# Performance work log

Hardware: AMD Instinct MI355X
Metric: run time of the kernel (lower is better)

Reference implementation:

```python
import jax, jax.numpy as jnp
import numpy as np

DIM = 256; HEADS = 8; B = 8; N = 128; MLP_HID = 4 * DIM


def _ln(x, g, b):
    m = x.mean(-1, keepdims=True)
    v = ((x - m) ** 2).mean(-1, keepdims=True)
    return (x - m) / jnp.sqrt(v + 1e-5) * g + b


def _mlp(x, W1, b1, W2, b2):
    return jax.nn.relu(x @ W1 + b1) @ W2 + b2


def setup_inputs():
    key = jax.random.key(0)
    ks = iter(jax.random.split(key, 48))
    def p(*shape):
        return jax.random.normal(next(ks), shape, jnp.float32) * 0.02
    inp = {
        'x': jax.random.normal(next(ks), (B, N, DIM), jnp.float32),
        'y': jax.random.normal(next(ks), (B, N, N, DIM), jnp.float32),
        'heads': HEADS,
    }
    for nm in ['q', 'k', 'v', 'e', 'oe', 'on']:
        inp['W' + nm] = p(DIM, DIM)
        inp['b' + nm] = p(DIM)
    for nm in ['ln1', 'ln3', 'ln4', 'ln5', 'ln6']:
        inp[nm + '_g'] = jnp.ones((DIM,), jnp.float32)
        inp[nm + '_b'] = jnp.zeros((DIM,), jnp.float32)
    inp['m1_W1'] = p(DIM, MLP_HID); inp['m1_b1'] = p(MLP_HID)
    inp['m1_W2'] = p(MLP_HID, DIM); inp['m1_b2'] = p(DIM)
    inp['m2_W1'] = p(DIM, MLP_HID); inp['m2_b1'] = p(MLP_HID)
    inp['m2_W2'] = p(MLP_HID, DIM); inp['m2_b2'] = p(DIM)
    return inp


def reference(x, y, heads, Wq, bq, Wk, bk, Wv, bv, We, be, Woe, boe, Won, bon,
              ln1_g, ln1_b, ln3_g, ln3_b, ln4_g, ln4_b, ln5_g, ln5_b, ln6_g, ln6_b,
              m1_W1, m1_b1, m1_W2, m1_b2, m2_W1, m2_b1, m2_W2, m2_b2):
    b, n, c = x.shape
    dk = c // heads
    x1 = _ln(x, ln1_g, ln1_b)
    q = (x1 @ Wq + bq).reshape(b, n, heads, dk)
    k = (x1 @ Wk + bk).reshape(b, n, heads, dk)
    v = (x1 @ Wv + bv).reshape(b, n, heads, dk)
    e = (y @ We + be).reshape(b, n, n, heads, dk)
    # elementwise QK (not a dot product), edge-modulated: (b,n,n,h,dk)
    attn = (q[:, :, None] * k[:, None]) / jnp.sqrt(jnp.float32(dk))
    attn = attn * (e + 1.0) * e
    edge = attn.reshape(b, n, n, c) @ Woe + boe
    attn = jax.nn.softmax(attn, axis=2)  # softmax over key/node axis
    node = (attn * v[:, None]).sum(axis=2).reshape(b, n, c)
    node = node @ Won + bon
    x2 = _ln(x1 + node, ln3_g, ln3_b)
    y2 = _ln(edge + y, ln4_g, ln4_b)
    x_out = _ln(x2 + _mlp(x2, m1_W1, m1_b1, m1_W2, m1_b2), ln5_g, ln5_b)
    y_out = _ln(y2 + _mlp(y2, m2_W1, m2_b1, m2_W2, m2_b2), ln6_g, ln6_b)
    return (x_out, y_out)
```

## Files before the change

kernel.cpp:

```cpp
#include <hip/hip_runtime.h>
#include <hip/hip_bf16.h>


#define DIMC 256
#define NSEQ 128
#define NB 8
#define HID 1024
#define EROWS (NB * NSEQ * NSEQ)

typedef __attribute__((ext_vector_type(8)))  short short8;
typedef __attribute__((ext_vector_type(16))) float f32x16;
typedef __attribute__((ext_vector_type(4)))  float f32x4;

__device__ __forceinline__ short f2bf(float f) {
    union { float f; unsigned u; } v; v.f = f;
    unsigned r = (v.u + 0x7FFF + ((v.u >> 16) & 1)) >> 16;
    return (short)r;
}
__device__ __forceinline__ float bf2f(short s) {
    union { unsigned u; float f; } v; v.u = ((unsigned)(unsigned short)s) << 16;
    return v.f;
}

__device__ __forceinline__ float wave_sum(float v) {
    #pragma unroll
    for (int o = 32; o; o >>= 1) v += __shfl_xor(v, o, 64);
    return v;
}

__device__ __forceinline__ float block_reduce_sum(float v, float* sc, int t) {
    #pragma unroll
    for (int o = 32; o > 0; o >>= 1) v += __shfl_down(v, o, 64);
    __syncthreads();
    if ((t & 63) == 0) sc[t >> 6] = v;
    __syncthreads();
    return sc[0] + sc[1] + sc[2] + sc[3];
}

__global__ __launch_bounds__(256, 2) void k_ln_qkv(
    const float* __restrict__ X, const float* __restrict__ g, const float* __restrict__ be,
    const float* __restrict__ Wq, const float* __restrict__ bq,
    const float* __restrict__ Wk, const float* __restrict__ bk,
    const float* __restrict__ Wv, const float* __restrict__ bv,
    float* __restrict__ X1, float* __restrict__ Q, float* __restrict__ K, float* __restrict__ V)
{
    __shared__ float xs[DIMC];
    __shared__ float red[4];
    const int t = threadIdx.x;
    const int row = blockIdx.x;
    float v = X[(size_t)row * DIMC + t];
    float mu = block_reduce_sum(v, red, t) * (1.f / DIMC);
    float d = v - mu;
    float var = block_reduce_sum(d * d, red, t) * (1.f / DIMC);
    float x1v = d * rsqrtf(var + 1e-5f) * g[t] + be[t];
    xs[t] = x1v;
    X1[(size_t)row * DIMC + t] = x1v;
    __syncthreads();
    float aq = bq[t], ak = bk[t], av = bv[t];
    #pragma unroll 4
    for (int k2 = 0; k2 < DIMC; ++k2) {
        float xv = xs[k2];
        aq = fmaf(xv, Wq[k2 * DIMC + t], aq);
        ak = fmaf(xv, Wk[k2 * DIMC + t], ak);
        av = fmaf(xv, Wv[k2 * DIMC + t], av);
    }
    Q[(size_t)row * DIMC + t] = aq;
    K[(size_t)row * DIMC + t] = ak;
    V[(size_t)row * DIMC + t] = av;
}

__global__ __launch_bounds__(256) void k_transpose_bf16(
    const float* __restrict__ src, short* __restrict__ dst, int M, int N)
{
    __shared__ short tile[32][33];
    const int t = threadIdx.x, tx = t & 31, ty = t >> 5;
    const int bx = blockIdx.x, by = blockIdx.y;
    #pragma unroll
    for (int r = ty; r < 32; r += 8)
        tile[r][tx] = f2bf(src[(size_t)(by * 32 + r) * N + bx * 32 + tx]);
    __syncthreads();
    #pragma unroll
    for (int r = ty; r < 32; r += 8)
        dst[(size_t)(bx * 32 + r) * M + by * 32 + tx] = tile[tx][r];
}

__global__ __launch_bounds__(256) void k_prep_wc(
    const float* __restrict__ W1, const float* __restrict__ W2, short* __restrict__ Wc)
{
    const int h = blockIdx.x, t = threadIdx.x;
    short* dst = Wc + (size_t)h * 32768;
    const int hh = t & 63, kq = t >> 6;
    for (int k0 = 0; k0 < 256; k0 += 4) {
        const int k = k0 + kq;
        float v = W1[(size_t)k * HID + h * 64 + hh];
        dst[hh * 256 + (((k >> 3) ^ (hh & 7)) << 3) + (k & 7)] = f2bf(v);
    }
    short* dst2 = dst + 16384;
    for (int kk = 0; kk < 64; ++kk) {
        float v = W2[(size_t)(h * 64 + kk) * DIMC + t];
        dst2[t * 64 + (((kk >> 3) ^ (t & 7)) << 3) + (kk & 7)] = f2bf(v);
    }
}

__global__ __launch_bounds__(256, 2) void k_e_attn_m(
    const float* __restrict__ Y, const short* __restrict__ WeT,
    const float* __restrict__ be,
    const float* __restrict__ Q, const float* __restrict__ Kp,
    short* __restrict__ ATTb)
{
    __shared__ __align__(16) short As[64][256];
    const int t = threadIdx.x, w = t >> 6, lane = t & 63;
    const int l31 = lane & 31, kg = lane >> 5;
    const size_t R0 = (size_t)blockIdx.x * 64;

    for (int r = w * 16; r < w * 16 + 16; ++r) {
        float4 y4 = *(const float4*)&Y[(R0 + r) * DIMC + lane * 4];
        short4 s4;
        s4.x = f2bf(y4.x); s4.y = f2bf(y4.y); s4.z = f2bf(y4.z); s4.w = f2bf(y4.w);
        *(short4*)&As[r][(((lane >> 1) ^ (r & 7)) << 3) + (lane & 1) * 4] = s4;
    }
    __syncthreads();

    const int rh = (w & 1) * 32, cbase = (w >> 1) * 128;
    const int sw = l31 & 7;
    f32x16 acc[4];
    #pragma unroll
    for (int a = 0; a < 4; ++a)
        #pragma unroll
        for (int i = 0; i < 16; ++i) acc[a][i] = 0.f;

    #pragma unroll
    for (int ks = 0; ks < 16; ++ks) {
        const int gk = 2 * ks + kg;
        short8 a = *(const short8*)&As[rh + l31][(gk ^ sw) * 8];
        #pragma unroll
        for (int tt = 0; tt < 4; ++tt) {
            short8 b = *(const short8*)&WeT[(size_t)(cbase + tt * 32 + l31) * DIMC + gk * 8];
            acc[tt] = __builtin_amdgcn_mfma_f32_32x32x16_bf16(a, b, acc[tt], 0, 0, 0);
        }
    }

    const int m0 = (int)(R0);
    const int qrow = m0 >> 7, bidx = m0 >> 14, jb = m0 & 127;
    const float isq = 0.17677669529663687f;
    #pragma unroll
    for (int tt = 0; tt < 4; ++tt) {
        const int n = cbase + tt * 32 + l31;
        const float qv = Q[(size_t)qrow * DIMC + n];
        const float bb = be[n];
        #pragma unroll
        for (int i = 0; i < 16; ++i) {
            const int row = rh + 4 * kg + (i & 3) + 8 * (i >> 2);
            const float kv = Kp[(size_t)((bidx << 7) + jb + row) * DIMC + n];
            const float e = acc[tt][i] + bb;
            const float qk = qv * kv * isq;
            ATTb[(size_t)(m0 + row) * DIMC + n] = f2bf(qk * (e + 1.f) * e);
        }
    }
}

__global__ __launch_bounds__(256, 2) void k_edge_m(
    const short* __restrict__ ATTb, const short* __restrict__ WoeT,
    const float* __restrict__ boe, float* __restrict__ EDGE)
{
    __shared__ __align__(16) short As[64][256];
    const int t = threadIdx.x, w = t >> 6, lane = t & 63;
    const int l31 = lane & 31, kg = lane >> 5;
    const size_t R0 = (size_t)blockIdx.x * 64;

    #pragma unroll
    for (int it = 0; it < 8; ++it) {
        const int r = w * 16 + it * 2 + kg;
        short8 v = *(const short8*)&ATTb[(R0 + r) * DIMC + l31 * 8];
        *(short8*)&As[r][((l31 ^ (r & 7))) * 8] = v;
    }
    __syncthreads();

    const int rh = (w & 1) * 32, cbase = (w >> 1) * 128;
    const int sw = l31 & 7;
    f32x16 acc[4];
    #pragma unroll
    for (int a = 0; a < 4; ++a)
        #pragma unroll
        for (int i = 0; i < 16; ++i) acc[a][i] = 0.f;

    #pragma unroll
    for (int ks = 0; ks < 16; ++ks) {
        const int gk = 2 * ks + kg;
        short8 a = *(const short8*)&As[rh + l31][(gk ^ sw) * 8];
        #pragma unroll
        for (int tt = 0; tt < 4; ++tt) {
            short8 b = *(const short8*)&WoeT[(size_t)(cbase + tt * 32 + l31) * DIMC + gk * 8];
            acc[tt] = __builtin_amdgcn_mfma_f32_32x32x16_bf16(a, b, acc[tt], 0, 0, 0);
        }
    }

    const int m0 = (int)(R0);
    #pragma unroll
    for (int tt = 0; tt < 4; ++tt) {
        const int n = cbase + tt * 32 + l31;
        const float bb = boe[n];
        #pragma unroll
        for (int i = 0; i < 16; ++i) {
            const int row = rh + 4 * kg + (i & 3) + 8 * (i >> 2);
            EDGE[(size_t)(m0 + row) * DIMC + n] = acc[tt][i] + bb;
        }
    }
}

__global__ __launch_bounds__(256, 2) void k_node_x(
    const short* __restrict__ ATTb, const float* __restrict__ V,
    const float* __restrict__ X1,
    const float* __restrict__ Won, const float* __restrict__ bon,
    const float* __restrict__ g3, const float* __restrict__ b3,
    const float* __restrict__ W1, const float* __restrict__ b1,
    const float* __restrict__ W2, const float* __restrict__ b2,
    const float* __restrict__ g5, const float* __restrict__ b5,
    float* __restrict__ OUTX)
{
    __shared__ float ns[DIMC];
    __shared__ float x2s[DIMC];
    __shared__ float hs[HID];
    __shared__ float red[4];
    const int t = threadIdx.x;
    const int bi = blockIdx.x;
    const int b = bi >> 7;
    const short* arow = ATTb + (size_t)bi * NSEQ * DIMC + t;
    const float* vbase = V + (size_t)b * NSEQ * DIMC + t;
    float l = 0.f, acc = 0.f;
    #pragma unroll 4
    for (int j = 0; j < NSEQ; ++j) {
        float a = bf2f(arow[(size_t)j * DIMC]);
        float vv = vbase[(size_t)j * DIMC];
        float p = __expf(a);
        l += p;
        acc = fmaf(p, vv, acc);
    }
    ns[t] = acc / l;
    __syncthreads();
    float o = bon[t];
    #pragma unroll 4
    for (int k2 = 0; k2 < DIMC; ++k2) o = fmaf(ns[k2], Won[k2 * DIMC + t], o);
    float resid = X1[(size_t)bi * DIMC + t] + o;
    float mu = block_reduce_sum(resid, red, t) * (1.f / DIMC);
    float d = resid - mu;
    float var = block_reduce_sum(d * d, red, t) * (1.f / DIMC);
    float x2 = d * rsqrtf(var + 1e-5f) * g3[t] + b3[t];
    x2s[t] = x2;
    __syncthreads();
    float4 h = *(const float4*)&b1[t * 4];
    for (int k2 = 0; k2 < DIMC; ++k2) {
        float xv = x2s[k2];
        float4 w = *(const float4*)&W1[(size_t)k2 * HID + t * 4];
        h.x = fmaf(xv, w.x, h.x); h.y = fmaf(xv, w.y, h.y);
        h.z = fmaf(xv, w.z, h.z); h.w = fmaf(xv, w.w, h.w);
    }
    h.x = fmaxf(h.x, 0.f); h.y = fmaxf(h.y, 0.f); h.z = fmaxf(h.z, 0.f); h.w = fmaxf(h.w, 0.f);
    *(float4*)&hs[t * 4] = h;
    __syncthreads();
    float o2 = b2[t];
    #pragma unroll 4
    for (int hh = 0; hh < HID; ++hh) o2 = fmaf(hs[hh], W2[(size_t)hh * DIMC + t], o2);
    float r2 = x2 + o2;
    float mu2 = block_reduce_sum(r2, red, t) * (1.f / DIMC);
    float d2 = r2 - mu2;
    float v2 = block_reduce_sum(d2 * d2, red, t) * (1.f / DIMC);
    OUTX[(size_t)bi * DIMC + t] = d2 * rsqrtf(v2 + 1e-5f) * g5[t] + b5[t];
}

__global__ __launch_bounds__(256, 1) void k_mlp_y6(
    float* __restrict__ EY, const float* __restrict__ Y,
    const float* __restrict__ g4, const float* __restrict__ b4,
    const short* __restrict__ Wc, const float* __restrict__ b1v,
    const float* __restrict__ b2v,
    const float* __restrict__ g6, const float* __restrict__ b6)
{
    __shared__ __align__(16) short Wbuf[2][32768];
    __shared__ __align__(16) short Hscr[4][32][64];
    const int t = threadIdx.x;
    const int w = t >> 6, lane = t & 63;
    const int l31 = lane & 31, kg = lane >> 5;
    const int r7 = l31 & 7;
    const size_t R0 = (size_t)blockIdx.x * 128;
    short* Wb = &Wbuf[0][0];

    {
        const float4 gv = *(const float4*)&g4[lane * 4];
        const float4 bv = *(const float4*)&b4[lane * 4];
        const int gw = lane >> 1;
        for (int rr = 0; rr < 32; ++rr) {
            const int row = w * 32 + rr;
            const float4 e4 = *(const float4*)&EY[(R0 + row) * DIMC + lane * 4];
            const float4 y4v = *(const float4*)&Y[(R0 + row) * DIMC + lane * 4];
            float v0 = e4.x + y4v.x, v1 = e4.y + y4v.y, v2 = e4.z + y4v.z, v3 = e4.w + y4v.w;
            float mu = wave_sum(v0 + v1 + v2 + v3) * (1.f / DIMC);
            float d0 = v0 - mu, d1 = v1 - mu, d2 = v2 - mu, d3 = v3 - mu;
            float var = wave_sum(d0 * d0 + d1 * d1 + d2 * d2 + d3 * d3) * (1.f / DIMC);
            float rs = rsqrtf(var + 1e-5f);
            short4 s4;
            s4.x = f2bf(d0 * rs * gv.x + bv.x);
            s4.y = f2bf(d1 * rs * gv.y + bv.y);
            s4.z = f2bf(d2 * rs * gv.z + bv.z);
            s4.w = f2bf(d3 * rs * gv.w + bv.w);
            *(short4*)&Wb[row * 256 + ((gw ^ (rr & 7)) << 3) + (lane & 1) * 4] = s4;
        }
    }
    short8 af[16];
    {
        const int row = w * 32 + l31;
        #pragma unroll
        for (int s = 0; s < 16; ++s)
            af[s] = *(const short8*)&Wb[row * 256 + (((2 * s + kg) ^ r7) << 3)];
    }

    auto stage = [&](int h, int buf) {
        const char* src = (const char*)Wc + (size_t)h * 65536 + t * 16;
        char* dstb = (char*)&Wbuf[buf][0] + t * 16;
        #pragma unroll
        for (int p = 0; p < 16; ++p) {
            __builtin_amdgcn_global_load_lds(
                (const __attribute__((address_space(1))) unsigned*)(src + p * 4096),
                (__attribute__((address_space(3))) unsigned*)(dstb + p * 4096),
                16, 0, 0);
        }
    };
    stage(0, 1);
    __syncthreads();

    f32x16 acc[8];
    #pragma unroll
    for (int a = 0; a < 8; ++a)
        #pragma unroll
        for (int i = 0; i < 16; ++i) acc[a][i] = 0.f;

    for (int h = 0; h < 16; ++h) {
        const short* Wlds = &Wbuf[1 - (h & 1)][0];
        if (h < 15) stage(h + 1, h & 1);
        const float bb0 = b1v[h * 64 + l31];
        const float bb1 = b1v[h * 64 + 32 + l31];

        f32x16 c1[2];
        #pragma unroll
        for (int a = 0; a < 2; ++a)
            #pragma unroll
            for (int i = 0; i < 16; ++i) c1[a][i] = 0.f;
        #pragma unroll
        for (int s = 0; s < 16; ++s) {
            const int g = ((2 * s + kg) ^ r7) << 3;
            #pragma unroll
            for (int tt = 0; tt < 2; ++tt) {
                short8 b = *(const short8*)&Wlds[(tt * 32 + l31) * 256 + g];
                c1[tt] = __builtin_amdgcn_mfma_f32_32x32x16_bf16(af[s], b, c1[tt], 0, 0, 0);
            }
        }
        #pragma unroll
        for (int tt = 0; tt < 2; ++tt) {
            const int cq = tt * 4 + (l31 >> 3), c7 = l31 & 7;
            const float bb = tt ? bb1 : bb0;
            #pragma unroll
            for (int i = 0; i < 16; ++i) {
                const int row = 4 * kg + (i & 3) + 8 * (i >> 2);
                Hscr[w][row][((cq ^ (row & 7)) << 3) + c7] =
                    f2bf(fmaxf(c1[tt][i] + bb, 0.f));
            }
        }
        #pragma unroll
        for (int s = 0; s < 4; ++s) {
            const int g2 = ((2 * s + kg) ^ r7) << 3;
            short8 hf = *(const short8*)&Hscr[w][l31][g2];
            #pragma unroll
            for (int ct = 0; ct < 8; ++ct) {
                short8 b = *(const short8*)&Wlds[16384 + (ct * 32 + l31) * 64 + g2];
                acc[ct] = __builtin_amdgcn_mfma_f32_32x32x16_bf16(hf, b, acc[ct], 0, 0, 0);
            }
        }
        __syncthreads();
    }

    {
        const int row = w * 32 + l31;
        #pragma unroll
        for (int s = 0; s < 16; ++s)
            *(short8*)&Wb[row * 256 + (((2 * s + kg) ^ r7) << 3)] = af[s];
    }
    #pragma unroll
    for (int ct = 0; ct < 8; ++ct) {
        const int col = ct * 32 + l31;
        const float bb = b2v[col];
        const int cq = col >> 3, c7 = col & 7;
        #pragma unroll
        for (int i = 0; i < 16; ++i) {
            const int row = 4 * kg + (i & 3) + 8 * (i >> 2);
            short yv = Wb[(w * 32 + row) * 256 + ((cq ^ (row & 7)) << 3) + c7];
            acc[ct][i] += bb + bf2f(yv);
        }
    }
    float mus[16], rss[16];
    #pragma unroll
    for (int i = 0; i < 16; ++i) {
        float s = 0.f;
        #pragma unroll
        for (int ct = 0; ct < 8; ++ct) s += acc[ct][i];
        #pragma unroll
        for (int m = 1; m < 32; m <<= 1) s += __shfl_xor(s, m, 64);
        mus[i] = s * (1.f / DIMC);
    }
    #pragma unroll
    for (int i = 0; i < 16; ++i) {
        float v = 0.f;
        #pragma unroll
        for (int ct = 0; ct < 8; ++ct) { float d = acc[ct][i] - mus[i]; v += d * d; }
        #pragma unroll
        for (int m = 1; m < 32; m <<= 1) v += __shfl_xor(v, m, 64);
        rss[i] = rsqrtf(v * (1.f / DIMC) + 1e-5f);
    }
    #pragma unroll
    for (int ct = 0; ct < 8; ++ct) {
        const int col = ct * 32 + l31;
        const float gg = g6[col], bo = b6[col];
        #pragma unroll
        for (int i = 0; i < 16; ++i) {
            const int row = 4 * kg + (i & 3) + 8 * (i >> 2);
            EY[(R0 + w * 32 + row) * DIMC + col] = (acc[ct][i] - mus[i]) * rss[i] * gg + bo;
        }
    }
}

extern "C" void kernel_launch(void* const* d_in, const int* in_sizes, int n_in,
                              void* d_out, int out_size, void* d_ws, size_t ws_size,
                              hipStream_t stream) {
    const float* x    = (const float*)d_in[0];
    const float* y    = (const float*)d_in[1];
    const float* Wq   = (const float*)d_in[3];  const float* bq  = (const float*)d_in[4];
    const float* Wk   = (const float*)d_in[5];  const float* bk  = (const float*)d_in[6];
    const float* Wv   = (const float*)d_in[7];  const float* bv  = (const float*)d_in[8];
    const float* We   = (const float*)d_in[9];  const float* be  = (const float*)d_in[10];
    const float* Woe  = (const float*)d_in[11]; const float* boe = (const float*)d_in[12];
    const float* Won  = (const float*)d_in[13]; const float* bon = (const float*)d_in[14];
    const float* ln1g = (const float*)d_in[15]; const float* ln1b = (const float*)d_in[16];
    const float* ln3g = (const float*)d_in[17]; const float* ln3b = (const float*)d_in[18];
    const float* ln4g = (const float*)d_in[19]; const float* ln4b = (const float*)d_in[20];
    const float* ln5g = (const float*)d_in[21]; const float* ln5b = (const float*)d_in[22];
    const float* ln6g = (const float*)d_in[23]; const float* ln6b = (const float*)d_in[24];
    const float* m1W1 = (const float*)d_in[25]; const float* m1b1 = (const float*)d_in[26];
    const float* m1W2 = (const float*)d_in[27]; const float* m1b2 = (const float*)d_in[28];
    const float* m2W1 = (const float*)d_in[29]; const float* m2b1 = (const float*)d_in[30];
    const float* m2W2 = (const float*)d_in[31]; const float* m2b2 = (const float*)d_in[32];

    float* outx = (float*)d_out;
    float* outy = (float*)d_out + NB * NSEQ * DIMC;

    float* ws  = (float*)d_ws;
    float* X1  = ws;
    float* Q   = ws + 262144;
    float* K   = ws + 524288;
    float* V   = ws + 786432;
    short* wsS = (short*)(ws + 1048576);
    short* WeT  = wsS;
    short* WoeT = wsS + 65536;
    short* Wc   = wsS + 131072;
    short* ATTb = wsS + 655360;

    k_transpose_bf16<<<dim3(8, 8),  256, 0, stream>>>(We,   WeT,  DIMC, DIMC);
    k_transpose_bf16<<<dim3(8, 8),  256, 0, stream>>>(Woe,  WoeT, DIMC, DIMC);
    k_prep_wc<<<16, 256, 0, stream>>>(m2W1, m2W2, Wc);

    k_ln_qkv<<<NB * NSEQ, 256, 0, stream>>>(x, ln1g, ln1b, Wq, bq, Wk, bk, Wv, bv, X1, Q, K, V);
    k_e_attn_m<<<EROWS / 64, 256, 0, stream>>>(y, WeT, be, Q, K, ATTb);
    k_edge_m<<<EROWS / 64, 256, 0, stream>>>(ATTb, WoeT, boe, outy);
    k_node_x<<<NB * NSEQ, 256, 0, stream>>>(ATTb, V, X1, Won, bon, ln3g, ln3b,
                                            m1W1, m1b1, m1W2, m1b2, ln5g, ln5b, outx);
    k_mlp_y6<<<EROWS / 128, 256, 0, stream>>>(outy, y, ln4g, ln4b,
                                              Wc, m2b1, m2b2, ln6g, ln6b);
}
```

Baseline: 1.077 ms.

## Halve LDS in edge MLP kernel to fit two blocks per CU

The edge-MLP kernel's full double buffer of combined W1/W2 chunks (128KB) is replaced by one W1 buffer and one W2 buffer (64KB total). Staging is reordered: W2 for the current chunk loads during the first GEMM, and W1 for the next chunk loads during the second GEMM. A barrier is added in between. Launch bounds rise to two blocks per CU to raise occupancy and hide latency, at the cost of less prefetch distance and an extra synchronization per iteration.

```diff
diff --git a/kernel.cpp b/kernel.cpp
--- a/kernel.cpp
+++ b/kernel.cpp
@@ -268,21 +268,21 @@
     OUTX[(size_t)bi * DIMC + t] = d2 * rsqrtf(v2 + 1e-5f) * g5[t] + b5[t];
 }
 
-__global__ __launch_bounds__(256, 1) void k_mlp_y6(
+__global__ __launch_bounds__(256, 2) void k_mlp_y7(
     float* __restrict__ EY, const float* __restrict__ Y,
     const float* __restrict__ g4, const float* __restrict__ b4,
     const short* __restrict__ Wc, const float* __restrict__ b1v,
     const float* __restrict__ b2v,
     const float* __restrict__ g6, const float* __restrict__ b6)
 {
-    __shared__ __align__(16) short Wbuf[2][32768];
+    __shared__ __align__(16) short Hbuf[2][16384];
     __shared__ __align__(16) short Hscr[4][32][64];
     const int t = threadIdx.x;
     const int w = t >> 6, lane = t & 63;
     const int l31 = lane & 31, kg = lane >> 5;
     const int r7 = l31 & 7;
     const size_t R0 = (size_t)blockIdx.x * 128;
-    short* Wb = &Wbuf[0][0];
+    short* Wb = &Hbuf[0][0];
 
     {
         const float4 gv = *(const float4*)&g4[lane * 4];
@@ -312,19 +312,32 @@
         for (int s = 0; s < 16; ++s)
             af[s] = *(const short8*)&Wb[row * 256 + (((2 * s + kg) ^ r7) << 3)];
     }
-
-    auto stage = [&](int h, int buf) {
+    __syncthreads();
+
+    auto stageW1 = [&](int h) {
         const char* src = (const char*)Wc + (size_t)h * 65536 + t * 16;
-        char* dstb = (char*)&Wbuf[buf][0] + t * 16;
-        #pragma unroll
-        for (int p = 0; p < 16; ++p) {
+        char* dstb = (char*)&Hbuf[0][0] + t * 16;
+        #pragma unroll
+        for (int p = 0; p < 8; ++p) {
             __builtin_amdgcn_global_load_lds(
                 (const __attribute__((address_space(1))) unsigned*)(src + p * 4096),
                 (__attribute__((address_space(3))) unsigned*)(dstb + p * 4096),
                 16, 0, 0);
         }
     };
-    stage(0, 1);
+    auto stageW2 = [&](int h) {
+        const char* src = (const char*)Wc + (size_t)h * 65536 + 32768 + t * 16;
+        char* dstb = (char*)&Hbuf[1][0] + t * 16;
+        #pragma unroll
+        for (int p = 0; p < 8; ++p) {
+            __builtin_amdgcn_global_load_lds(
+                (const __attribute__((address_space(1))) unsigned*)(src + p * 4096),
+                (__attribute__((address_space(3))) unsigned*)(dstb + p * 4096),
+                16, 0, 0);
+        }
+    };
+
+    stageW1(0);
     __syncthreads();
 
     f32x16 acc[8];
@@ -334,11 +347,9 @@
         for (int i = 0; i < 16; ++i) acc[a][i] = 0.f;
 
     for (int h = 0; h < 16; ++h) {
-        const short* Wlds = &Wbuf[1 - (h & 1)][0];
-        if (h < 15) stage(h + 1, h & 1);
+        stageW2(h);
         const float bb0 = b1v[h * 64 + l31];
         const float bb1 = b1v[h * 64 + 32 + l31];
-
         f32x16 c1[2];
         #pragma unroll
         for (int a = 0; a < 2; ++a)
@@ -349,7 +360,7 @@
             const int g = ((2 * s + kg) ^ r7) << 3;
             #pragma unroll
             for (int tt = 0; tt < 2; ++tt) {
-                short8 b = *(const short8*)&Wlds[(tt * 32 + l31) * 256 + g];
+                short8 b = *(const short8*)&Hbuf[0][(tt * 32 + l31) * 256 + g];
                 c1[tt] = __builtin_amdgcn_mfma_f32_32x32x16_bf16(af[s], b, c1[tt], 0, 0, 0);
             }
         }
@@ -364,13 +375,16 @@
                     f2bf(fmaxf(c1[tt][i] + bb, 0.f));
             }
         }
+        __syncthreads();
+
+        if (h < 15) stageW1(h + 1);
         #pragma unroll
         for (int s = 0; s < 4; ++s) {
             const int g2 = ((2 * s + kg) ^ r7) << 3;
             short8 hf = *(const short8*)&Hscr[w][l31][g2];
             #pragma unroll
             for (int ct = 0; ct < 8; ++ct) {
-                short8 b = *(const short8*)&Wlds[16384 + (ct * 32 + l31) * 64 + g2];
+                short8 b = *(const short8*)&Hbuf[1][(ct * 32 + l31) * 64 + g2];
                 acc[ct] = __builtin_amdgcn_mfma_f32_32x32x16_bf16(hf, b, acc[ct], 0, 0, 0);
             }
         }
@@ -470,6 +484,6 @@
     k_edge_m<<<EROWS / 64, 256, 0, stream>>>(ATTb, WoeT, boe, outy);
     k_node_x<<<NB * NSEQ, 256, 0, stream>>>(ATTb, V, X1, Won, bon, ln3g, ln3b,
                                             m1W1, m1b1, m1W2, m1b2, ln5g, ln5b, outx);
-    k_mlp_y6<<<EROWS / 128, 256, 0, stream>>>(outy, y, ln4g, ln4b,
+    k_mlp_y7<<<EROWS / 128, 256, 0, stream>>>(outy, y, ln4g, ln4b,
                                               Wc, m2b1, m2b2, ln6g, ln6b);
 }
```

New measurement: 972.7 us. -9.7%, faster.
